# Optimization experiments

Measured on AMD Instinct MI355X. Metric: run time of the kernel, lower is better.

## Reference

```python
import jax, jax.numpy as jnp
import numpy as np
import math

B, L, D, NUM_TYPES = 4, 4096, 512, 22
T_MAX = 200.0
SIGMA, LAMBD = 10.0, 0.005


def setup_inputs() -> dict:
    key = jax.random.key(0)
    k1, k2, k3 = jax.random.split(key, 3)
    event_type = jax.random.randint(k1, (B, L), 0, NUM_TYPES + 1)
    # event times in [0, t_max), sorted along the sequence (realistic point process)
    event_time = jnp.sort(jax.random.uniform(k2, (B, L), dtype=jnp.float32) * T_MAX, axis=-1)
    # embedding table with padding row 0 zeroed (padding_idx=0)
    emb_table = jax.random.normal(k3, (NUM_TYPES + 1, D), dtype=jnp.float32).at[0].set(0.0)
    return {"event_type": event_type, "event_time": event_time, "emb_table": emb_table}


def reference(event_type, event_time, emb_table):
    d_model = emb_table.shape[1]
    seq_len = event_time.shape[1]

    # sinusoidal temporal encoding: t / 10000^(2*(i//2)/d)
    i = jnp.arange(d_model)
    pos_vec = jnp.power(jnp.float32(10000.0), 2.0 * (i // 2).astype(jnp.float32) / d_model)
    temp = event_time[:, :, None] / pos_vec  # [B, L, D]
    temp_enc = jnp.where(i % 2 == 0, jnp.sin(temp), jnp.cos(temp))

    type_embedding = emb_table[event_type] * math.sqrt(d_model)  # [B, L, D]
    embedding = jnp.concatenate([temp_enc, type_embedding], axis=-1)  # [B, L, 2D]

    # RBF kernel pairwise scores: sigma^2 * exp(-(|ti - tj|^norm)^2 / lambd^2), norm=2
    t = event_time / T_MAX  # normalized times
    d = jnp.abs(t[:, :, None] - t[:, None, :]) ** 2  # [B, L, L]
    scores = (SIGMA ** 2) * jnp.exp(-(d ** 2) / (LAMBD ** 2))

    # causal mask: keep j <= i, fill future with -1000, then softmax over rows
    causal = jnp.tril(jnp.ones((seq_len, seq_len), dtype=bool))  # [L, L]
    scores = jnp.where(causal[None, :, :], scores, jnp.float32(-1000.0))
    scores = jax.nn.softmax(scores, axis=-1)
    return scores, embedding
```

## Files before the change

### kernel.cpp

```cpp
#include <hip/hip_runtime.h>

#define SEQ_L 4096
#define BATCH 4
#define DMODEL 512
#define CUT 0.055f
#define RPB 16
#define SCORE_BLOCKS (BATCH * SEQ_L / RPB)
#define EMB_BLOCKS 512
#define EMB_RPB (BATCH * SEQ_L / EMB_BLOCKS)

__global__ __launch_bounds__(256) void fused_kernel(const int* __restrict__ et,
                                                    const float* __restrict__ tm,
                                                    const float* __restrict__ tab,
                                                    float* __restrict__ scores,
                                                    float* __restrict__ emb) {
    if (blockIdx.x < SCORE_BLOCKS) {
        __shared__ float ts[SEQ_L];
        const int b  = blockIdx.x / (SEQ_L / RPB);
        const int i0 = (blockIdx.x % (SEQ_L / RPB)) * RPB;

        const float4* tb4 = (const float4*)(tm + b * SEQ_L);
        float4* ts4 = (float4*)ts;
        const float inv_tmax = 1.0f / 200.0f;
        #pragma unroll
        for (int q = 0; q < 4; ++q) {
            int j = threadIdx.x + q * 256;
            float4 v = tb4[j];
            v.x *= inv_tmax; v.y *= inv_tmax; v.z *= inv_tmax; v.w *= inv_tmax;
            ts4[j] = v;
        }
        __syncthreads();

        const int wave = threadIdx.x >> 6;
        const int lane = threadIdx.x & 63;
        const int ibase = i0 + wave * 4;

        int jlo;
        {
            const float tc = ts[ibase] - CUT;
            int lo = 0, hi = ibase;
            while (lo < hi) {
                int mid = (lo + hi) >> 1;
                if (ts[mid] < tc) lo = mid + 1; else hi = mid;
            }
            jlo = lo;
        }

        for (int r = 0; r < 4; ++r) {
            const int i = ibase + r;
            const float ti = ts[i];
            const float tc = ti - CUT;
            while (ts[jlo] < tc) ++jlo;

            float sum = 0.0f;
            for (int j = jlo + lane; j <= i; j += 64) {
                float d = ti - ts[j];
                float d2 = d * d;
                float s = 100.0f * __expf(-(d2 * d2) * 40000.0f);
                sum += __expf(s - 100.0f);
            }
            #pragma unroll
            for (int off = 1; off < 64; off <<= 1) sum += __shfl_xor(sum, off, 64);
            const float inv_denom = 1.0f / sum;

            float4* out4 = (float4*)(scores + ((size_t)(b * SEQ_L + i)) * SEQ_L);
            for (int c = lane; c < SEQ_L / 4; c += 64) {
                const int j = c * 4;
                float4 v = make_float4(0.0f, 0.0f, 0.0f, 0.0f);
                if (j + 3 >= jlo && j <= i) {
                    float* vp = &v.x;
                    #pragma unroll
                    for (int q = 0; q < 4; ++q) {
                        const int jj = j + q;
                        if (jj >= jlo && jj <= i) {
                            float d = ti - ts[jj];
                            float d2 = d * d;
                            float s = 100.0f * __expf(-(d2 * d2) * 40000.0f);
                            vp[q] = __expf(s - 100.0f) * inv_denom;
                        }
                    }
                }
                out4[c] = v;
            }
        }
    } else {
        const int t = threadIdx.x;
        const bool temporal = t < 128;

        float ipA = 0.0f, ipB = 0.0f;
        if (temporal) {
            const float c = -13.287712379549449f / 256.0f;
            ipA = exp2f(c * (float)(2 * t));
            ipB = exp2f(c * (float)(2 * t + 1));
        }
        const int ecol = (t - 128) * 4;

        const int bl0 = (blockIdx.x - SCORE_BLOCKS) * EMB_RPB;
        for (int r = 0; r < EMB_RPB; ++r) {
            const int bl = bl0 + r;
            float4 v;
            if (temporal) {
                const float time = tm[bl];
                const float a = time * ipA;
                const float bp = time * ipB;
                v.x = __sinf(a);  v.y = __cosf(a);
                v.z = __sinf(bp); v.w = __cosf(bp);
            } else {
                const float4 e = *(const float4*)(tab + et[bl] * DMODEL + ecol);
                const float sc = 22.627416997969522f;
                v.x = e.x * sc; v.y = e.y * sc; v.z = e.z * sc; v.w = e.w * sc;
            }
            ((float4*)(emb + (size_t)bl * 2 * DMODEL))[t] = v;
        }
    }
}

extern "C" void kernel_launch(void* const* d_in, const int* in_sizes, int n_in,
                              void* d_out, int out_size, void* d_ws, size_t ws_size,
                              hipStream_t stream) {
    const int*   event_type = (const int*)d_in[0];
    const float* event_time = (const float*)d_in[1];
    const float* emb_table  = (const float*)d_in[2];

    float* scores = (float*)d_out;
    float* emb    = scores + (size_t)BATCH * SEQ_L * SEQ_L;

    fused_kernel<<<SCORE_BLOCKS + EMB_BLOCKS, 256, 0, stream>>>(
        event_type, event_time, emb_table, scores, emb);
}
```

Before: 65.34 us.

## Use nontemporal stores, split zero/compute loops, ballot-based jlo scan, 8 rows per wave

```diff
diff --git a/kernel.cpp b/kernel.cpp
--- a/kernel.cpp
+++ b/kernel.cpp
@@ -4,10 +4,17 @@
 #define BATCH 4
 #define DMODEL 512
 #define CUT 0.055f
-#define RPB 16
+#define RPW 8
+#define RPB 32
 #define SCORE_BLOCKS (BATCH * SEQ_L / RPB)
 #define EMB_BLOCKS 512
 #define EMB_RPB (BATCH * SEQ_L / EMB_BLOCKS)
+
+typedef float f4 __attribute__((ext_vector_type(4)));
+
+__device__ __forceinline__ void nt_store4(f4* p, f4 v) {
+    __builtin_nontemporal_store(v, p);
+}
 
 __global__ __launch_bounds__(256) void fused_kernel(const int* __restrict__ et,
                                                     const float* __restrict__ tm,
@@ -19,21 +26,21 @@
         const int b  = blockIdx.x / (SEQ_L / RPB);
         const int i0 = (blockIdx.x % (SEQ_L / RPB)) * RPB;
 
-        const float4* tb4 = (const float4*)(tm + b * SEQ_L);
-        float4* ts4 = (float4*)ts;
-        const float inv_tmax = 1.0f / 200.0f;
+        const f4* tb4 = (const f4*)(tm + b * SEQ_L);
+        f4* ts4 = (f4*)ts;
         #pragma unroll
         for (int q = 0; q < 4; ++q) {
             int j = threadIdx.x + q * 256;
-            float4 v = tb4[j];
-            v.x *= inv_tmax; v.y *= inv_tmax; v.z *= inv_tmax; v.w *= inv_tmax;
-            ts4[j] = v;
+            ts4[j] = tb4[j] * (1.0f / 200.0f);
         }
         __syncthreads();
 
         const int wave = threadIdx.x >> 6;
         const int lane = threadIdx.x & 63;
-        const int ibase = i0 + wave * 4;
+        const int ibase = i0 + wave * RPW;
+
+        float tiR[RPW], invR[RPW];
+        int   jloR[RPW];
 
         int jlo;
         {
@@ -46,12 +53,17 @@
             jlo = lo;
         }
 
-        for (int r = 0; r < 4; ++r) {
+        #pragma unroll
+        for (int r = 0; r < RPW; ++r) {
             const int i = ibase + r;
             const float ti = ts[i];
             const float tc = ti - CUT;
-            while (ts[jlo] < tc) ++jlo;
-
+            for (;;) {
+                int idx = jlo + lane; if (idx > SEQ_L - 1) idx = SEQ_L - 1;
+                int cnt = __popcll(__ballot(ts[idx] < tc));
+                jlo += cnt;
+                if (cnt < 64) break;
+            }
             float sum = 0.0f;
             for (int j = jlo + lane; j <= i; j += 64) {
                 float d = ti - ts[j];
@@ -61,27 +73,36 @@
             }
             #pragma unroll
             for (int off = 1; off < 64; off <<= 1) sum += __shfl_xor(sum, off, 64);
-            const float inv_denom = 1.0f / sum;
+            tiR[r] = ti; invR[r] = 1.0f / sum; jloR[r] = jlo;
+        }
 
-            float4* out4 = (float4*)(scores + ((size_t)(b * SEQ_L + i)) * SEQ_L);
-            for (int c = lane; c < SEQ_L / 4; c += 64) {
-                const int j = c * 4;
-                float4 v = make_float4(0.0f, 0.0f, 0.0f, 0.0f);
-                if (j + 3 >= jlo && j <= i) {
-                    float* vp = &v.x;
-                    #pragma unroll
-                    for (int q = 0; q < 4; ++q) {
-                        const int jj = j + q;
-                        if (jj >= jlo && jj <= i) {
-                            float d = ti - ts[jj];
-                            float d2 = d * d;
-                            float s = 100.0f * __expf(-(d2 * d2) * 40000.0f);
-                            vp[q] = __expf(s - 100.0f) * inv_denom;
-                        }
-                    }
+        #pragma unroll
+        for (int r = 0; r < RPW; ++r) {
+            const int i = ibase + r;
+            const float ti = tiR[r], inv = invR[r];
+            const int jl = jloR[r];
+            const int c_lo = jl >> 2, c_hi = i >> 2;
+            f4* out4 = (f4*)(scores + ((size_t)(b * SEQ_L + i)) * SEQ_L);
+            const f4 z = {0.0f, 0.0f, 0.0f, 0.0f};
+
+            for (int c = lane; c < c_lo; c += 64)
+                nt_store4(out4 + c, z);
+            for (int c = c_lo + lane; c <= c_hi; c += 64) {
+                f4 tv = ts4[c];
+                f4 v;
+                #pragma unroll
+                for (int q = 0; q < 4; ++q) {
+                    const int jj = 4 * c + q;
+                    float d = ti - tv[q];
+                    float d2 = d * d;
+                    float s = 100.0f * __expf(-(d2 * d2) * 40000.0f);
+                    float p = __expf(s - 100.0f) * inv;
+                    v[q] = (jj >= jl && jj <= i) ? p : 0.0f;
                 }
-                out4[c] = v;
+                nt_store4(out4 + c, v);
             }
+            for (int c = c_hi + 1 + lane; c < SEQ_L / 4; c += 64)
+                nt_store4(out4 + c, z);
         }
     } else {
         const int t = threadIdx.x;
@@ -95,22 +116,21 @@
         }
         const int ecol = (t - 128) * 4;
 
-        const int bl0 = (blockIdx.x - SCORE_BLOCKS) * EMB_RPB;
+        const int bl0 = ((int)blockIdx.x - SCORE_BLOCKS) * EMB_RPB;
         for (int r = 0; r < EMB_RPB; ++r) {
             const int bl = bl0 + r;
-            float4 v;
+            f4 v;
             if (temporal) {
                 const float time = tm[bl];
                 const float a = time * ipA;
                 const float bp = time * ipB;
-                v.x = __sinf(a);  v.y = __cosf(a);
-                v.z = __sinf(bp); v.w = __cosf(bp);
+                v[0] = __sinf(a);  v[1] = __cosf(a);
+                v[2] = __sinf(bp); v[3] = __cosf(bp);
             } else {
-                const float4 e = *(const float4*)(tab + et[bl] * DMODEL + ecol);
-                const float sc = 22.627416997969522f;
-                v.x = e.x * sc; v.y = e.y * sc; v.z = e.z * sc; v.w = e.w * sc;
+                f4 e = *(const f4*)(tab + et[bl] * DMODEL + ecol);
+                v = e * 22.627416997969522f;
             }
-            ((float4*)(emb + (size_t)bl * 2 * DMODEL))[t] = v;
+            nt_store4((f4*)(emb + (size_t)bl * 2 * DMODEL) + t, v);
         }
     }
 }
```

After: 78.11 us. +19.5%, slower.
